# Performance work log

Hardware: AMD Instinct MI355X
Metric: run time of the kernel (lower is better)

Reference implementation:

```python
import jax, jax.numpy as jnp
import numpy as np

B, N = 32, 256
PHI1, PHI2 = 64, 128
RHO1, RHO2, OUT = 256, 128, 64


def setup_inputs() -> dict:
    key = jax.random.key(0)
    ks = jax.random.split(key, 12)
    dm = jax.random.normal(ks[0], (B, N, N), dtype=jnp.float32)
    lengths = jnp.clip(jax.random.randint(ks[1], (B,), 0, N), 2, N).astype(jnp.int32)

    def lin(k, fan_in, fan_out):
        # torch nn.Linear default init: U(-1/sqrt(fan_in), 1/sqrt(fan_in))
        bound = 1.0 / np.sqrt(fan_in)
        kw, kb = jax.random.split(k)
        W = jax.random.uniform(kw, (fan_in, fan_out), jnp.float32, -bound, bound)
        b = jax.random.uniform(kb, (fan_out,), jnp.float32, -bound, bound)
        return W, b

    W1, b1 = lin(ks[2], 1, PHI1)
    W2, b2 = lin(ks[3], PHI1, PHI2)
    W3, b3 = lin(ks[4], PHI2, RHO1)
    W4, b4 = lin(ks[5], RHO1, RHO2)
    W5, b5 = lin(ks[6], RHO2, OUT)
    return {"dm": dm, "lengths": lengths, "W1": W1, "b1": b1, "W2": W2, "b2": b2,
            "W3": W3, "b3": b3, "W4": W4, "b4": b4, "W5": W5, "b5": b5}


def reference(dm, lengths, W1, b1, W2, b2, W3, b3, W4, b4, W5, b5):
    # Static upper-triangular (offset=1) index pairs: P = N*(N-1)/2
    iu0, iu1 = jnp.triu_indices(N, k=1)
    scalars = dm[:, iu0, iu1]                                   # [B, P]
    # Ragged mask: a pair (i, j) exists only if both indices < item length
    mask = (iu0[None, :] < lengths[:, None]) & (iu1[None, :] < lengths[:, None])  # [B, P]
    # phi MLP applied per scalar: 1 -> 64 -> 128, ReLU after each
    h = jax.nn.relu(scalars[..., None] * W1[0] + b1)            # [B, P, 64]
    h = jax.nn.relu(jnp.einsum('bpd,de->bpe', h, W2) + b2)      # [B, P, 128]
    # Masked sum-pool over pairs
    pooled = jnp.sum(h * mask[..., None].astype(h.dtype), axis=1)  # [B, 128]
    # rho MLP: 128 -> 256 -> 128 -> OUT (ReLU on hidden layers only)
    r = jax.nn.relu(pooled @ W3 + b3)
    r = jax.nn.relu(r @ W4 + b4)
    return r @ W5 + b5                                           # [B, OUT]
```

## Files before the change

kernel.cpp:

```cpp
#include <hip/hip_runtime.h>
#include <hip/hip_bf16.h>


#define NB 32
#define NN 256
#define PHI2 128
#define SEGS 65

__global__ __launch_bounds__(128) void build_tables(
    const float* __restrict__ W1, const float* __restrict__ b1,
    const float* __restrict__ W2, const float* __restrict__ b2,
    float4* __restrict__ table4,
    float* __restrict__ tsort, float* __restrict__ pooled) {
  __shared__ float w2_s[64 * PHI2];
  __shared__ float t_s[64], w1_s[64], b1_s[64];
  __shared__ float a_sh[128], b_sh[128];
  __shared__ int cat_s[64], rank_s[64];
  const int tid = threadIdx.x;
  const int seg = blockIdx.x;
  const float4* W2v = (const float4*)W2;
  float4* w2v = (float4*)w2_s;
  for (int i = tid; i < 64 * PHI2 / 4; i += 128) w2v[i] = W2v[i];
  if (tid < 64) {
    float w = W1[tid], bb = b1[tid];
    w1_s[tid] = w; b1_s[tid] = bb;
    int cat; float t;
    if (w > 0.f)      { cat = 0; t = -bb / w; }
    else if (w < 0.f) { cat = 1; t = -bb / w; }
    else              { cat = (bb > 0.f) ? 2 : 3; t = 0.f; }
    t_s[tid] = t; cat_s[tid] = cat;
  }
  __syncthreads();
  if (tid < 64) {
    float t = t_s[tid]; int r = 0;
    for (int k = 0; k < 64; ++k) {
      float tk = t_s[k];
      r += (tk < t) || (tk == t && k < tid);
    }
    rank_s[tid] = r;
    if (seg == 0) tsort[r] = t;
  }
  __syncthreads();
  float a = 0.f, bsum = b2[tid];
#pragma unroll 8
  for (int j = 0; j < 64; ++j) {
    int cat = cat_s[j], r = rank_s[j];
    bool act = (cat == 0) ? (seg > r) : (cat == 1) ? (seg <= r) : (cat == 2);
    float w2 = w2_s[j * PHI2 + tid];
    float m = act ? 1.f : 0.f;
    a    = fmaf(m * w1_s[j], w2, a);
    bsum = fmaf(m * b1_s[j], w2, bsum);
  }
  a_sh[tid] = a; b_sh[tid] = bsum;
  __syncthreads();
  if (tid < 64)
    table4[seg * 64 + tid] =
        make_float4(a_sh[tid], b_sh[tid], a_sh[tid + 64], b_sh[tid + 64]);
  if (seg == 0) {
    for (int i = tid; i < NB * PHI2; i += 128) pooled[i] = 0.f;
  }
}

__global__ __launch_bounds__(512) void phi_pool(
    const float* __restrict__ dm, const int* __restrict__ lengths,
    const float4* __restrict__ table4, const float* __restrict__ tsort,
    float* __restrict__ pooled) {
  __shared__ float4 ab_s[SEGS * 64];
  const int chunk = blockIdx.x;
  const int b     = blockIdx.y;
  const int tid = threadIdx.x;
  const int lane = tid & 63, w = tid >> 6;

  const int len = lengths[b];
  if (chunk * 8 >= len - 1) return;

  for (int i = tid; i < SEGS * 64; i += 512) ab_s[i] = table4[i];
  __syncthreads();

  const float tv = tsort[lane];
  const float* dmb = dm + (size_t)b * (NN * NN);
  float acc0 = 0.f, acc1 = 0.f;

  for (int i0 = chunk * 8 + w; i0 < len - 1; i0 += 128) {
    const float* row = dmb + i0 * NN + i0 + 1;
    const int cnt_total = len - 1 - i0;
    float sv = (lane < cnt_total) ? row[lane] : 0.f;
    for (int base = 0; base < cnt_total; base += 64) {
      const int cnt = min(64, cnt_total - base);
      const int nb = base + 64;
      float svn = 0.f;
      if (nb < cnt_total && lane < cnt_total - nb) svn = row[nb + lane];
      if (cnt == 64) {
#pragma unroll 8
        for (int j = 0; j < 64; ++j) {
          float s = __int_as_float(__builtin_amdgcn_readlane(__float_as_int(sv), j));
          int pos = (int)__popcll(__ballot(tv < s));
          float4 p = ab_s[pos * 64 + lane];
          acc0 += fmaxf(fmaf(p.x, s, p.y), 0.f);
          acc1 += fmaxf(fmaf(p.z, s, p.w), 0.f);
        }
      } else {
        for (int j = 0; j < cnt; ++j) {
          float s = __int_as_float(__builtin_amdgcn_readlane(__float_as_int(sv), j));
          int pos = (int)__popcll(__ballot(tv < s));
          float4 p = ab_s[pos * 64 + lane];
          acc0 += fmaxf(fmaf(p.x, s, p.y), 0.f);
          acc1 += fmaxf(fmaf(p.z, s, p.w), 0.f);
        }
      }
      sv = svn;
    }
  }
  atomicAdd(&pooled[b * PHI2 + lane], acc0);
  atomicAdd(&pooled[b * PHI2 + 64 + lane], acc1);
}

__global__ __launch_bounds__(256) void rho_mlp(
    const float* __restrict__ pooled,
    const float* __restrict__ W3, const float* __restrict__ b3,
    const float* __restrict__ W4, const float* __restrict__ b4,
    const float* __restrict__ W5, const float* __restrict__ b5,
    float* __restrict__ out) {
  __shared__ float w_s[128 * 256];
  __shared__ float p_s[128], r1_s[256], r2_s[128];
  const int b = blockIdx.x, tid = threadIdx.x;
  float4* wsv = (float4*)w_s;
  {
    const float4* w3v = (const float4*)W3;
    for (int i = tid; i < 8192; i += 256) wsv[i] = w3v[i];
  }
  if (tid < 128) p_s[tid] = pooled[b * 128 + tid];
  __syncthreads();
  {
    float acc = b3[tid];
#pragma unroll 8
    for (int k = 0; k < 128; ++k) acc = fmaf(p_s[k], w_s[k * 256 + tid], acc);
    r1_s[tid] = fmaxf(acc, 0.f);
  }
  __syncthreads();
  {
    const float4* w4v = (const float4*)W4;
    for (int i = tid; i < 8192; i += 256) wsv[i] = w4v[i];
  }
  __syncthreads();
  if (tid < 128) {
    float acc = b4[tid];
#pragma unroll 8
    for (int k = 0; k < 256; ++k) acc = fmaf(r1_s[k], w_s[k * 128 + tid], acc);
    r2_s[tid] = fmaxf(acc, 0.f);
  }
  __syncthreads();
  {
    const float4* w5v = (const float4*)W5;
    for (int i = tid; i < 2048; i += 256) wsv[i] = w5v[i];
  }
  __syncthreads();
  if (tid < 64) {
    float acc = b5[tid];
#pragma unroll 8
    for (int k = 0; k < 128; ++k) acc = fmaf(r2_s[k], w_s[k * 64 + tid], acc);
    out[b * 64 + tid] = acc;
  }
}

extern "C" void kernel_launch(void* const* d_in, const int* in_sizes, int n_in,
                              void* d_out, int out_size, void* d_ws, size_t ws_size,
                              hipStream_t stream) {
  const float* dm      = (const float*)d_in[0];
  const int*   lengths = (const int*)d_in[1];
  const float* W1 = (const float*)d_in[2];
  const float* b1 = (const float*)d_in[3];
  const float* W2 = (const float*)d_in[4];
  const float* b2 = (const float*)d_in[5];
  const float* W3 = (const float*)d_in[6];
  const float* b3 = (const float*)d_in[7];
  const float* W4 = (const float*)d_in[8];
  const float* b4 = (const float*)d_in[9];
  const float* W5 = (const float*)d_in[10];
  const float* b5 = (const float*)d_in[11];

  float* ws = (float*)d_ws;
  float4* table4 = (float4*)ws;
  float* tsort   = ws + 16640;
  float* pooled  = ws + 16704;

  build_tables<<<SEGS, 128, 0, stream>>>(W1, b1, W2, b2, table4, tsort, pooled);
  phi_pool<<<dim3(16, NB), 512, 0, stream>>>(dm, lengths, table4, tsort, pooled);
  rho_mlp<<<NB, 256, 0, stream>>>(pooled, W3, b3, W4, b4, W5, b5, (float*)d_out);
}
```

Baseline: 142.9 us.

## Split phi_pool over output halves and pair triangle rows for balance

Adds a grid dimension that splits the 128 phi outputs into two halves. Each block now loads only a float2 table (half the LDS) and keeps one accumulator, which doubles the block count. Row assignment changes from strided to pairing row r with row 254-r, so every block gets roughly equal triangle work. The cost is that every block recomputes the ballot/popcount segment search for its half, duplicating that work across the two halves.

```diff
diff --git a/kernel.cpp b/kernel.cpp
--- a/kernel.cpp
+++ b/kernel.cpp
@@ -10,11 +10,10 @@
 __global__ __launch_bounds__(128) void build_tables(
     const float* __restrict__ W1, const float* __restrict__ b1,
     const float* __restrict__ W2, const float* __restrict__ b2,
-    float4* __restrict__ table4,
+    float2* __restrict__ table2,
     float* __restrict__ tsort, float* __restrict__ pooled) {
   __shared__ float w2_s[64 * PHI2];
   __shared__ float t_s[64], w1_s[64], b1_s[64];
-  __shared__ float a_sh[128], b_sh[128];
   __shared__ int cat_s[64], rank_s[64];
   const int tid = threadIdx.x;
   const int seg = blockIdx.x;
@@ -51,37 +50,41 @@
     a    = fmaf(m * w1_s[j], w2, a);
     bsum = fmaf(m * b1_s[j], w2, bsum);
   }
-  a_sh[tid] = a; b_sh[tid] = bsum;
-  __syncthreads();
-  if (tid < 64)
-    table4[seg * 64 + tid] =
-        make_float4(a_sh[tid], b_sh[tid], a_sh[tid + 64], b_sh[tid + 64]);
+  const int h = tid >> 6, l = tid & 63;
+  table2[((h * SEGS) + seg) * 64 + l] = make_float2(a, bsum);
   if (seg == 0) {
     for (int i = tid; i < NB * PHI2; i += 128) pooled[i] = 0.f;
   }
 }
 
-__global__ __launch_bounds__(512) void phi_pool(
+__global__ __launch_bounds__(512, 8) void phi_pool(
     const float* __restrict__ dm, const int* __restrict__ lengths,
-    const float4* __restrict__ table4, const float* __restrict__ tsort,
+    const float2* __restrict__ table2, const float* __restrict__ tsort,
     float* __restrict__ pooled) {
-  __shared__ float4 ab_s[SEGS * 64];
+  __shared__ float2 ab_s[SEGS * 64];
   const int chunk = blockIdx.x;
-  const int b     = blockIdx.y;
+  const int h     = blockIdx.y;
+  const int b     = blockIdx.z;
   const int tid = threadIdx.x;
   const int lane = tid & 63, w = tid >> 6;
 
   const int len = lengths[b];
-  if (chunk * 8 >= len - 1) return;
+  if (8 * chunk > len - 2 && 247 - 8 * chunk > len - 2) return;
 
-  for (int i = tid; i < SEGS * 64; i += 512) ab_s[i] = table4[i];
+  const float2* tg = table2 + h * SEGS * 64;
+  for (int i = tid; i < SEGS * 64; i += 512) ab_s[i] = tg[i];
   __syncthreads();
 
   const float tv = tsort[lane];
   const float* dmb = dm + (size_t)b * (NN * NN);
-  float acc0 = 0.f, acc1 = 0.f;
+  float acc = 0.f;
 
-  for (int i0 = chunk * 8 + w; i0 < len - 1; i0 += 128) {
+  const int r1 = chunk * 8 + w;
+#pragma unroll
+  for (int t = 0; t < 2; ++t) {
+    const int i0 = (t == 0) ? r1 : 254 - r1;
+    if (t == 1 && i0 == r1) continue;
+    if (i0 > len - 2) continue;
     const float* row = dmb + i0 * NN + i0 + 1;
     const int cnt_total = len - 1 - i0;
     float sv = (lane < cnt_total) ? row[lane] : 0.f;
@@ -95,24 +98,21 @@
         for (int j = 0; j < 64; ++j) {
           float s = __int_as_float(__builtin_amdgcn_readlane(__float_as_int(sv), j));
           int pos = (int)__popcll(__ballot(tv < s));
-          float4 p = ab_s[pos * 64 + lane];
-          acc0 += fmaxf(fmaf(p.x, s, p.y), 0.f);
-          acc1 += fmaxf(fmaf(p.z, s, p.w), 0.f);
+          float2 p = ab_s[pos * 64 + lane];
+          acc += fmaxf(fmaf(p.x, s, p.y), 0.f);
         }
       } else {
         for (int j = 0; j < cnt; ++j) {
           float s = __int_as_float(__builtin_amdgcn_readlane(__float_as_int(sv), j));
           int pos = (int)__popcll(__ballot(tv < s));
-          float4 p = ab_s[pos * 64 + lane];
-          acc0 += fmaxf(fmaf(p.x, s, p.y), 0.f);
-          acc1 += fmaxf(fmaf(p.z, s, p.w), 0.f);
+          float2 p = ab_s[pos * 64 + lane];
+          acc += fmaxf(fmaf(p.x, s, p.y), 0.f);
         }
       }
       sv = svn;
     }
   }
-  atomicAdd(&pooled[b * PHI2 + lane], acc0);
-  atomicAdd(&pooled[b * PHI2 + 64 + lane], acc1);
+  atomicAdd(&pooled[b * PHI2 + h * 64 + lane], acc);
 }
 
 __global__ __launch_bounds__(256) void rho_mlp(
@@ -180,11 +180,11 @@
   const float* b5 = (const float*)d_in[11];
 
   float* ws = (float*)d_ws;
-  float4* table4 = (float4*)ws;
+  float2* table2 = (float2*)ws;
   float* tsort   = ws + 16640;
   float* pooled  = ws + 16704;
 
-  build_tables<<<SEGS, 128, 0, stream>>>(W1, b1, W2, b2, table4, tsort, pooled);
-  phi_pool<<<dim3(16, NB), 512, 0, stream>>>(dm, lengths, table4, tsort, pooled);
+  build_tables<<<SEGS, 128, 0, stream>>>(W1, b1, W2, b2, table2, tsort, pooled);
+  phi_pool<<<dim3(16, 2, NB), 512, 0, stream>>>(dm, lengths, table2, tsort, pooled);
   rho_mlp<<<NB, 256, 0, stream>>>(pooled, W3, b3, W4, b4, W5, b5, (float*)d_out);
 }
```

After: 132.9 us. -7.0%, faster.

## Pair complementary triangle rows per wave and split columns across block halves

Applied to the files above, without the earlier changes.

Reassigns phi_pool work so each wave handles row i and its complement 254-i, balancing the triangular pair count. Each block half processes alternating 4-column groups, and the block grows to 1024 threads. Each row is loaded once as a float4 per lane and individual values are broadcast via readlane. This adds branchy edge handling and bigger blocks that may limit occupancy, plus duplicate table loads into LDS per block.

```diff
diff --git a/kernel.cpp b/kernel.cpp
--- a/kernel.cpp
+++ b/kernel.cpp
@@ -61,56 +61,79 @@
   }
 }
 
-__global__ __launch_bounds__(512) void phi_pool(
+__device__ __forceinline__ void visit(float comp, int L, float tv, int lane,
+                                      const float4* ab_s, float& acc0,
+                                      float& acc1) {
+  float s = __int_as_float(__builtin_amdgcn_readlane(__float_as_int(comp), L));
+  int pos = (int)__popcll(__ballot(tv < s));
+  float4 p = ab_s[pos * 64 + lane];
+  acc0 += fmaxf(fmaf(p.x, s, p.y), 0.f);
+  acc1 += fmaxf(fmaf(p.z, s, p.w), 0.f);
+}
+
+__device__ __forceinline__ void visit_dyn(const float4& f4, int j, float tv,
+                                          int lane, const float4* ab_s,
+                                          float& acc0, float& acc1) {
+  int c = j & 3;
+  float comp = (c == 0) ? f4.x : (c == 1) ? f4.y : (c == 2) ? f4.z : f4.w;
+  visit(comp, j >> 2, tv, lane, ab_s, acc0, acc1);
+}
+
+__device__ __forceinline__ void do_row(const float4& f4, int i0, int len,
+                                       int half, float tv, int lane,
+                                       const float4* ab_s, float& acc0,
+                                       float& acc1) {
+  const int jlo = i0 + 1, jhi = len - 1;
+  const int fullLo = (jlo + 3) >> 2;
+  const int fullHi = (jhi >= 3) ? ((jhi - 3) >> 2) : -1;
+  if (fullLo > fullHi) {
+    for (int j = jlo; j <= jhi; ++j)
+      if (((j >> 2) & 1) == half) visit_dyn(f4, j, tv, lane, ab_s, acc0, acc1);
+    return;
+  }
+  for (int j = jlo; j < fullLo * 4; ++j)
+    if (((j >> 2) & 1) == half) visit_dyn(f4, j, tv, lane, ab_s, acc0, acc1);
+  int L0 = fullLo + (((fullLo & 1) != half) ? 1 : 0);
+#pragma unroll 2
+  for (int L = L0; L <= fullHi; L += 2) {
+    visit(f4.x, L, tv, lane, ab_s, acc0, acc1);
+    visit(f4.y, L, tv, lane, ab_s, acc0, acc1);
+    visit(f4.z, L, tv, lane, ab_s, acc0, acc1);
+    visit(f4.w, L, tv, lane, ab_s, acc0, acc1);
+  }
+  for (int j = fullHi * 4 + 4; j <= jhi; ++j)
+    if (((j >> 2) & 1) == half) visit_dyn(f4, j, tv, lane, ab_s, acc0, acc1);
+}
+
+__global__ __launch_bounds__(1024, 8) void phi_pool(
     const float* __restrict__ dm, const int* __restrict__ lengths,
     const float4* __restrict__ table4, const float* __restrict__ tsort,
     float* __restrict__ pooled) {
   __shared__ float4 ab_s[SEGS * 64];
-  const int chunk = blockIdx.x;
+  const int c_row = blockIdx.x >> 1;
+  const int half  = blockIdx.x & 1;
   const int b     = blockIdx.y;
   const int tid = threadIdx.x;
   const int lane = tid & 63, w = tid >> 6;
 
   const int len = lengths[b];
-  if (chunk * 8 >= len - 1) return;
-
-  for (int i = tid; i < SEGS * 64; i += 512) ab_s[i] = table4[i];
+  if (c_row * 16 > len - 2 && 239 - c_row * 16 > len - 2) return;
+
+  for (int i = tid; i < SEGS * 64; i += 1024) ab_s[i] = table4[i];
   __syncthreads();
 
   const float tv = tsort[lane];
   const float* dmb = dm + (size_t)b * (NN * NN);
   float acc0 = 0.f, acc1 = 0.f;
 
-  for (int i0 = chunk * 8 + w; i0 < len - 1; i0 += 128) {
-    const float* row = dmb + i0 * NN + i0 + 1;
-    const int cnt_total = len - 1 - i0;
-    float sv = (lane < cnt_total) ? row[lane] : 0.f;
-    for (int base = 0; base < cnt_total; base += 64) {
-      const int cnt = min(64, cnt_total - base);
-      const int nb = base + 64;
-      float svn = 0.f;
-      if (nb < cnt_total && lane < cnt_total - nb) svn = row[nb + lane];
-      if (cnt == 64) {
-#pragma unroll 8
-        for (int j = 0; j < 64; ++j) {
-          float s = __int_as_float(__builtin_amdgcn_readlane(__float_as_int(sv), j));
-          int pos = (int)__popcll(__ballot(tv < s));
-          float4 p = ab_s[pos * 64 + lane];
-          acc0 += fmaxf(fmaf(p.x, s, p.y), 0.f);
-          acc1 += fmaxf(fmaf(p.z, s, p.w), 0.f);
-        }
-      } else {
-        for (int j = 0; j < cnt; ++j) {
-          float s = __int_as_float(__builtin_amdgcn_readlane(__float_as_int(sv), j));
-          int pos = (int)__popcll(__ballot(tv < s));
-          float4 p = ab_s[pos * 64 + lane];
-          acc0 += fmaxf(fmaf(p.x, s, p.y), 0.f);
-          acc1 += fmaxf(fmaf(p.z, s, p.w), 0.f);
-        }
-      }
-      sv = svn;
-    }
-  }
+  const int rA = c_row * 16 + w;
+  const int rB = 254 - rA;
+  const float4 fA = ((const float4*)(dmb + rA * NN))[lane];
+  const float4 fB = ((const float4*)(dmb + rB * NN))[lane];
+  if (rA <= len - 2) do_row(fA, rA, len, half, tv, lane, ab_s, acc0, acc1);
+  if (rB != rA && rB <= len - 2)
+    do_row(fB, rB, len, half, tv, lane, ab_s, acc0, acc1);
+
   atomicAdd(&pooled[b * PHI2 + lane], acc0);
   atomicAdd(&pooled[b * PHI2 + 64 + lane], acc1);
 }
@@ -185,6 +208,6 @@
   float* pooled  = ws + 16704;
 
   build_tables<<<SEGS, 128, 0, stream>>>(W1, b1, W2, b2, table4, tsort, pooled);
-  phi_pool<<<dim3(16, NB), 512, 0, stream>>>(dm, lengths, table4, tsort, pooled);
+  phi_pool<<<dim3(16, NB), 1024, 0, stream>>>(dm, lengths, table4, tsort, pooled);
   rho_mlp<<<NB, 256, 0, stream>>>(pooled, W3, b3, W4, b4, W5, b5, (float*)d_out);
 }
```

Measured after the change: 133.3 us. 6.8% less time.
